# Kernel tuning notes

Measured on AMD Instinct MI355X. Metric: run time of the kernel, lower is better.

The kernel has to match this reference:

```python
import jax, jax.numpy as jnp
import numpy as np

B, T, A, IN = 128, 512, 2, 192
N_SESS, RDIM, OUT = 512, 64, 256


def setup_inputs() -> dict:
    key = jax.random.key(0)
    k1, k2, k3, k4 = jax.random.split(key, 4)
    state_in = jax.random.normal(k1, (B, T, A, IN), dtype=jnp.float32)
    session = jax.random.randint(k2, (B,), 0, N_SESS, dtype=jnp.int64)
    # kaiming-uniform-like init scale, exact distribution irrelevant for correctness baseline
    unique_readin = jax.random.normal(k3, (N_SESS, IN, RDIM), dtype=jnp.float32) * (1.0 / np.sqrt(IN))
    project = jax.random.normal(k4, (RDIM, OUT), dtype=jnp.float32) * (1.0 / np.sqrt(RDIM))
    return {"state_in": state_in, "session": session,
            "unique_readin": unique_readin, "project": project}


def reference(state_in, session, unique_readin, project):
    # gather per-sample readin matrices: [B, IN, RDIM]
    readin_matrix = unique_readin[session]
    # btai,bih->btah : per-sample matmul over the input-feature axis
    h = jnp.einsum('btai,bih->btah', state_in, readin_matrix)
    # low-rank compression projection to model dim: [B, T, A, OUT]
    out = jnp.matmul(h, project)
    return out
```

## Files before the change

kernel.cpp:

```cpp
#include <hip/hip_runtime.h>
#include <hip/hip_bf16.h>
#include <stdint.h>


typedef short    bf16x8 __attribute__((ext_vector_type(8)));
typedef float    f32x4  __attribute__((ext_vector_type(4)));
typedef uint32_t u32x4  __attribute__((ext_vector_type(4)));

#define NB    128
#define MPB   1024
#define INF   192
#define RDIM  64
#define OUTF  256

__device__ __forceinline__ uint16_t f2bf(float f) {
    union { float f; uint32_t u; } v; v.f = f;
    return (uint16_t)((v.u + 0x7fffu + ((v.u >> 16) & 1u)) >> 16);
}
__device__ __forceinline__ uint32_t pack2(float a, float b) {
    return (uint32_t)f2bf(a) | ((uint32_t)f2bf(b) << 16);
}

__device__ __forceinline__ bf16x8 cvt8(f32x4 a, f32x4 b) {
    union { __hip_bfloat162 h2[4]; bf16x8 h; } r;
    r.h2[0] = __float22bfloat162_rn({a[0], a[1]});
    r.h2[1] = __float22bfloat162_rn({a[2], a[3]});
    r.h2[2] = __float22bfloat162_rn({b[0], b[1]});
    r.h2[3] = __float22bfloat162_rn({b[2], b[3]});
    return r.h;
}

__device__ __forceinline__ void gl_lds16(const void* g, void* l) {
    auto gp = (const __attribute__((address_space(1))) uint32_t*)(uintptr_t)g;
    auto lp = (__attribute__((address_space(3))) uint32_t*)(uintptr_t)l;
    __builtin_amdgcn_global_load_lds(gp, lp, 16, 0, 0);
}

__global__ __launch_bounds__(256) void k1_build_w(
    const float* __restrict__ readin,
    const float* __restrict__ project,
    const int*   __restrict__ session,
    uint16_t*    __restrict__ Wt)
{
    __shared__ uint16_t Rl[INF * 64];
    __shared__ uint16_t Pl[128 * 64];

    const int b  = blockIdx.x >> 1;
    const int oh = blockIdx.x & 1;
    const int t  = threadIdx.x;
    const float* Rg = readin + (size_t)session[b] * (INF * RDIM);

#pragma unroll
    for (int c = 0; c < 3; ++c) {
        int idx = c * 4096 + t * 16;
        int row = idx >> 6;
        int kg0 = (idx & 63) >> 3;
        f32x4 v0 = *(const f32x4*)(Rg + idx);
        f32x4 v1 = *(const f32x4*)(Rg + idx + 4);
        f32x4 v2 = *(const f32x4*)(Rg + idx + 8);
        f32x4 v3 = *(const f32x4*)(Rg + idx + 12);
        u32x4 d0, d1;
        d0[0] = pack2(v0[0], v0[1]); d0[1] = pack2(v0[2], v0[3]);
        d0[2] = pack2(v1[0], v1[1]); d0[3] = pack2(v1[2], v1[3]);
        d1[0] = pack2(v2[0], v2[1]); d1[1] = pack2(v2[2], v2[3]);
        d1[2] = pack2(v3[0], v3[1]); d1[3] = pack2(v3[2], v3[3]);
        *(u32x4*)&Rl[row * 64 + (((kg0    ) ^ (row & 7)) << 3)] = d0;
        *(u32x4*)&Rl[row * 64 + (((kg0 + 1) ^ (row & 7)) << 3)] = d1;
    }
    {
        int h  = t >> 2;
        int og = (t & 3) * 32;
        const float* Pg = project + (size_t)h * OUTF + oh * 128 + og;
#pragma unroll
        for (int q = 0; q < 8; ++q) {
            f32x4 v = *(const f32x4*)(Pg + q * 4);
#pragma unroll
            for (int e = 0; e < 4; ++e) {
                int o = og + q * 4 + e;
                Pl[o * 64 + (((h >> 3) ^ (o & 7)) << 3) + (h & 7)] = f2bf(v[e]);
            }
        }
    }
    __syncthreads();

    const int l  = t & 63, w = t >> 6;
    const int wm = w >> 1, wn = w & 1;
    const int lr = l & 15, lk = l >> 4;

    f32x4 acc[4][6];
#pragma unroll
    for (int m = 0; m < 4; ++m)
#pragma unroll
        for (int n = 0; n < 6; ++n) acc[m][n] = f32x4{0.f, 0.f, 0.f, 0.f};

#pragma unroll
    for (int kk = 0; kk < 2; ++kk) {
        int kg = kk * 4 + lk;
        bf16x8 a[4], bb[6];
#pragma unroll
        for (int m = 0; m < 4; ++m) {
            int row = wm * 64 + m * 16 + lr;
            a[m] = *(const bf16x8*)&Pl[row * 64 + ((kg ^ (row & 7)) << 3)];
        }
#pragma unroll
        for (int n = 0; n < 6; ++n) {
            int col = wn * 96 + n * 16 + lr;
            bb[n] = *(const bf16x8*)&Rl[col * 64 + ((kg ^ (col & 7)) << 3)];
        }
#pragma unroll
        for (int m = 0; m < 4; ++m)
#pragma unroll
            for (int n = 0; n < 6; ++n)
                acc[m][n] = __builtin_amdgcn_mfma_f32_16x16x32_bf16(
                    a[m], bb[n], acc[m][n], 0, 0, 0);
    }

    uint16_t* Wb = Wt + ((size_t)b * OUTF + oh * 128) * INF;
#pragma unroll
    for (int m = 0; m < 4; ++m) {
        int o = wm * 64 + m * 16 + lk * 4;
#pragma unroll
        for (int n = 0; n < 6; ++n) {
            int i = wn * 96 + n * 16 + lr;
#pragma unroll
            for (int j = 0; j < 4; ++j)
                Wb[(size_t)(o + j) * INF + i] = f2bf(acc[m][n][j]);
        }
    }
}

#define A_STRIDE 144
#define A_CHUNKS 18
#define B_CHUNKS 8

__global__ __launch_bounds__(256, 3) void k2_gemm(
    const float*    __restrict__ X,
    const uint16_t* __restrict__ Wt,
    float*          __restrict__ Y)
{
    __shared__ uint8_t  As[2][A_CHUNKS * 1024];
    __shared__ uint16_t Bs[2][B_CHUNKS * 512];

    const int bid0 = blockIdx.x;
    const int bid  = ((bid0 & 7) << 8) | (bid0 >> 3);
    const int b  = bid >> 4;
    const int mt = (bid >> 1) & 7;
    const int nt = bid & 1;
    const int t  = threadIdx.x, l = t & 63, w = t >> 6;

    const float*    Xb = X  + ((size_t)b * MPB  + mt * 128) * INF;
    const uint16_t* Wb = Wt + ((size_t)b * OUTF + nt * 128) * INF;
    float*          Yb = Y  + ((size_t)b * MPB  + mt * 128) * OUTF + nt * 128;

    int aoff[5];
    bool avalid[5];
    int achunk[5];
#pragma unroll
    for (int j = 0; j < 5; ++j) {
        int c = j * 4 + w;
        achunk[j] = c;
        avalid[j] = (c < A_CHUNKS);
        int u    = c * 64 + l;
        int row  = u / 9;
        int unit = u - row * 9;
        aoff[j] = row * INF + (unit < 8 ? unit * 4 : 0);
    }
    int boff[2];
#pragma unroll
    for (int j = 0; j < 2; ++j) {
        int c = j * 4 + w;
        boff[j] = (c * 16 + (l >> 2)) * INF + (l & 3) * 8;
    }

    auto stageA = [&](int ks, int buf) {
#pragma unroll
        for (int j = 0; j < 5; ++j)
            if (avalid[j])
                gl_lds16(Xb + aoff[j] + ks * 32, &As[buf][achunk[j] * 1024]);
    };
    auto stageB = [&](int ks, int buf) {
#pragma unroll
        for (int j = 0; j < 2; ++j)
            gl_lds16(Wb + boff[j] + ks * 32, &Bs[buf][(j * 4 + w) * 512]);
    };

    stageA(0, 0);
    stageB(0, 0);

    const int wm = w >> 1, wn = w & 1;
    const int lr = l & 15, lk = l >> 4;

    f32x4 acc[4][4];
#pragma unroll
    for (int m = 0; m < 4; ++m)
#pragma unroll
        for (int n = 0; n < 4; ++n) acc[m][n] = f32x4{0.f, 0.f, 0.f, 0.f};

    __syncthreads();

#pragma unroll
    for (int ks = 0; ks < 6; ++ks) {
        const int cur = ks & 1;
        if (ks < 5) { stageA(ks + 1, cur ^ 1); stageB(ks + 1, cur ^ 1); }

        bf16x8 af[4], bfr[4];
#pragma unroll
        for (int m = 0; m < 4; ++m) {
            int row = wm * 64 + m * 16 + lr;
            const uint8_t* p = &As[cur][row * A_STRIDE + lk * 32];
            f32x4 lo = *(const f32x4*)(p);
            f32x4 hi = *(const f32x4*)(p + 16);
            af[m] = cvt8(lo, hi);
        }
#pragma unroll
        for (int n = 0; n < 4; ++n) {
            int rn = wn * 64 + n * 16 + lr;
            bfr[n] = *(const bf16x8*)&Bs[cur][rn * 32 + lk * 8];
        }
#pragma unroll
        for (int m = 0; m < 4; ++m)
#pragma unroll
            for (int n = 0; n < 4; ++n)
                acc[m][n] = __builtin_amdgcn_mfma_f32_16x16x32_bf16(
                    af[m], bfr[n], acc[m][n], 0, 0, 0);

        __syncthreads();
    }

#pragma unroll
    for (int m = 0; m < 4; ++m) {
        int r0 = wm * 64 + m * 16 + lk * 4;
#pragma unroll
        for (int n = 0; n < 4; ++n) {
            int c0 = wn * 64 + n * 16 + lr;
#pragma unroll
            for (int j = 0; j < 4; ++j)
                Yb[(size_t)(r0 + j) * OUTF + c0] = acc[m][n][j];
        }
    }
}

extern "C" void kernel_launch(void* const* d_in, const int* in_sizes, int n_in,
                              void* d_out, int out_size, void* d_ws, size_t ws_size,
                              hipStream_t stream) {
    (void)in_sizes; (void)n_in; (void)out_size; (void)ws_size;
    const float* state   = (const float*)d_in[0];
    const int*   session = (const int*)  d_in[1];
    const float* readin  = (const float*)d_in[2];
    const float* project = (const float*)d_in[3];
    float*    out = (float*)d_out;
    uint16_t* Wt  = (uint16_t*)d_ws;

    hipLaunchKernelGGL(k1_build_w, dim3(256), dim3(256), 0, stream,
                       readin, project, session, Wt);
    hipLaunchKernelGGL(k2_gemm, dim3(2048), dim3(256), 0, stream,
                       state, Wt, out);
}
```

Before: 55.72 us.

## Triple-buffer GEMM staging with vmcnt waits and XOR-swizzled LDS layout

Switches the k2 GEMM from double to triple buffering, issuing loads two stages ahead and waiting on explicit vmcnt counts with a single barrier per step instead of two full syncthreads. The padded A layout (stride 144) and the B layout are replaced by XOR-swizzled 128-byte and 64-byte rows to avoid LDS bank conflicts without padding. Launch bounds drop to 2 blocks per CU because LDS use per block goes up, which lowers occupancy in return for deeper prefetch.

```diff
diff --git a/kernel.cpp b/kernel.cpp
--- a/kernel.cpp
+++ b/kernel.cpp
@@ -12,6 +12,9 @@
 #define INF   192
 #define RDIM  64
 #define OUTF  256
+
+#define WAIT_VM6() asm volatile("s_waitcnt vmcnt(6)" ::: "memory")
+#define WAIT_VM0() asm volatile("s_waitcnt vmcnt(0)" ::: "memory")
 
 __device__ __forceinline__ uint16_t f2bf(float f) {
     union { float f; uint32_t u; } v; v.f = f;
@@ -129,17 +132,13 @@
     }
 }
 
-#define A_STRIDE 144
-#define A_CHUNKS 18
-#define B_CHUNKS 8
-
-__global__ __launch_bounds__(256, 3) void k2_gemm(
+__global__ __launch_bounds__(256, 2) void k2_gemm(
     const float*    __restrict__ X,
     const uint16_t* __restrict__ Wt,
     float*          __restrict__ Y)
 {
-    __shared__ uint8_t  As[2][A_CHUNKS * 1024];
-    __shared__ uint16_t Bs[2][B_CHUNKS * 512];
+    __shared__ uint8_t  As[3][16384];
+    __shared__ uint16_t Bs[3][4096];
 
     const int bid0 = blockIdx.x;
     const int bid  = ((bid0 & 7) << 8) | (bid0 >> 3);
@@ -152,43 +151,36 @@
     const uint16_t* Wb = Wt + ((size_t)b * OUTF + nt * 128) * INF;
     float*          Yb = Y  + ((size_t)b * MPB  + mt * 128) * OUTF + nt * 128;
 
-    int aoff[5];
-    bool avalid[5];
-    int achunk[5];
-#pragma unroll
-    for (int j = 0; j < 5; ++j) {
-        int c = j * 4 + w;
-        achunk[j] = c;
-        avalid[j] = (c < A_CHUNKS);
-        int u    = c * 64 + l;
-        int row  = u / 9;
-        int unit = u - row * 9;
-        aoff[j] = row * INF + (unit < 8 ? unit * 4 : 0);
+    int aoff[4];
+#pragma unroll
+    for (int j = 0; j < 4; ++j) {
+        int c = w * 4 + j;
+        aoff[j] = (c * 8 + (l >> 3)) * INF + (((l & 7) ^ (l >> 3)) << 2);
     }
     int boff[2];
 #pragma unroll
     for (int j = 0; j < 2; ++j) {
-        int c = j * 4 + w;
-        boff[j] = (c * 16 + (l >> 2)) * INF + (l & 3) * 8;
-    }
-
-    auto stageA = [&](int ks, int buf) {
-#pragma unroll
-        for (int j = 0; j < 5; ++j)
-            if (avalid[j])
-                gl_lds16(Xb + aoff[j] + ks * 32, &As[buf][achunk[j] * 1024]);
+        int c = w * 2 + j;
+        boff[j] = (c * 16 + (l >> 2)) * INF + (((l & 3) ^ ((l >> 2) & 3)) << 3);
+    }
+
+    auto stage = [&](int ks, int buf) {
+#pragma unroll
+        for (int j = 0; j < 4; ++j)
+            gl_lds16(Xb + aoff[j] + ks * 32, &As[buf][(w * 4 + j) * 1024]);
+#pragma unroll
+        for (int j = 0; j < 2; ++j)
+            gl_lds16(Wb + boff[j] + ks * 32, &Bs[buf][(w * 2 + j) * 512]);
     };
-    auto stageB = [&](int ks, int buf) {
-#pragma unroll
-        for (int j = 0; j < 2; ++j)
-            gl_lds16(Wb + boff[j] + ks * 32, &Bs[buf][(j * 4 + w) * 512]);
-    };
-
-    stageA(0, 0);
-    stageB(0, 0);
+
+    stage(0, 0);
+    stage(1, 1);
 
     const int wm = w >> 1, wn = w & 1;
     const int lr = l & 15, lk = l >> 4;
+    const int as0 = (((2 * lk)     ^ (lr & 7)) << 4);
+    const int as1 = (((2 * lk + 1) ^ (lr & 7)) << 4);
+    const int bs0 = ((lk ^ (lr & 3)) << 4);
 
     f32x4 acc[4][4];
 #pragma unroll
@@ -196,26 +188,27 @@
 #pragma unroll
         for (int n = 0; n < 4; ++n) acc[m][n] = f32x4{0.f, 0.f, 0.f, 0.f};
 
-    __syncthreads();
-
 #pragma unroll
     for (int ks = 0; ks < 6; ++ks) {
-        const int cur = ks & 1;
-        if (ks < 5) { stageA(ks + 1, cur ^ 1); stageB(ks + 1, cur ^ 1); }
+        const int cur = ks % 3;
+        if (ks < 5) { WAIT_VM6(); } else { WAIT_VM0(); }
+        __builtin_amdgcn_s_barrier();
+        __builtin_amdgcn_sched_barrier(0);
+        if (ks < 4) stage(ks + 2, (ks + 2) % 3);
 
         bf16x8 af[4], bfr[4];
 #pragma unroll
         for (int m = 0; m < 4; ++m) {
             int row = wm * 64 + m * 16 + lr;
-            const uint8_t* p = &As[cur][row * A_STRIDE + lk * 32];
-            f32x4 lo = *(const f32x4*)(p);
-            f32x4 hi = *(const f32x4*)(p + 16);
+            const uint8_t* p = &As[cur][row * 128];
+            f32x4 lo = *(const f32x4*)(p + as0);
+            f32x4 hi = *(const f32x4*)(p + as1);
             af[m] = cvt8(lo, hi);
         }
 #pragma unroll
         for (int n = 0; n < 4; ++n) {
             int rn = wn * 64 + n * 16 + lr;
-            bfr[n] = *(const bf16x8*)&Bs[cur][rn * 32 + lk * 8];
+            bfr[n] = *(const bf16x8*)((const uint8_t*)&Bs[cur][0] + rn * 64 + bs0);
         }
 #pragma unroll
         for (int m = 0; m < 4; ++m)
@@ -223,8 +216,6 @@
             for (int n = 0; n < 4; ++n)
                 acc[m][n] = __builtin_amdgcn_mfma_f32_16x16x32_bf16(
                     af[m], bfr[n], acc[m][n], 0, 0, 0);
-
-        __syncthreads();
     }
 
 #pragma unroll
```

Result: faster. 54.04 us (-3.0%).
